# Performance work log

Measured on AMD Instinct MI355X. Metric: run time of the kernel, lower is better.

## Reference

```python
import jax, jax.numpy as jnp
import numpy as np

SQ, B, H, D = 2048, 1, 16, 64
HIDDEN = H * D


def setup_inputs() -> dict:
    key = jax.random.key(0)
    kq, kk, kv = jax.random.split(key, 3)
    query_layer = jax.random.normal(kq, (SQ, B, H, D), dtype=jnp.float32)
    key_layer = jax.random.normal(kk, (SQ, B, H, D), dtype=jnp.float32)
    value_layer = jax.random.normal(kv, (SQ, B, H, D), dtype=jnp.float32)
    return {"query_layer": query_layer, "key_layer": key_layer, "value_layer": value_layer}


def reference(query_layer, key_layer, value_layer):
    sq, b, h, d = query_layer.shape
    sk = key_layer.shape[0]
    norm = 1.0 / jnp.sqrt(jnp.asarray(d, dtype=query_layer.dtype))
    # scores: [b, h, sq, sk]  (materialized in the original via baddbmm)
    scores = jnp.einsum('sbhd,tbhd->bhst', query_layer, key_layer) * norm
    # causal mask (tril over [sq, sk]); masked positions -> -10000.0 as in original
    causal = jnp.tril(jnp.ones((sq, sk), dtype=bool))
    scores = jnp.where(causal[None, None], scores, jnp.asarray(-10000.0, scores.dtype))
    probs = jax.nn.softmax(scores, axis=-1)
    # context: [sq, b, h, d] -> [sq, b, hidden]
    ctx = jnp.einsum('bhst,tbhd->sbhd', probs, value_layer)
    return ctx.reshape(sq, b, h * d)
```

## Files before the change

kernel.cpp:

```cpp
#include <hip/hip_runtime.h>

typedef __bf16 bf16_t;
typedef bf16_t bf16x4 __attribute__((ext_vector_type(4)));
typedef bf16_t bf16x8 __attribute__((ext_vector_type(8)));
typedef float f32x4 __attribute__((ext_vector_type(4)));

namespace {
constexpr int kSQ = 2048;
constexpr int kNH = 16;
constexpr int kHD = 64;
constexpr int kHID = kNH * kHD;
constexpr int kBM = 64;
constexpr int kBN = 64;
constexpr int kPitch = 72;
constexpr int kNM = kSQ / kBM;
}

__global__ __launch_bounds__(256, 2)
void fattn_kernel(const float* __restrict__ Qg, const float* __restrict__ Kg,
                  const float* __restrict__ Vg, float* __restrict__ Og) {
  __shared__ __align__(16) bf16_t qs[kBM * kPitch];
  __shared__ __align__(16) bf16_t ks[kBN * kPitch];
  __shared__ __align__(16) bf16_t vt[kHD * kPitch];
  __shared__ __align__(16) bf16_t ps[4 * 16 * kPitch];

  const int bid  = blockIdx.x;
  const int head = bid & (kNH - 1);
  const int idx  = (bid >> 4) & 15;
  const int mblk = (bid < 256) ? (31 - idx) : idx;
  const int m0   = mblk * kBM;

  const int tid  = threadIdx.x;
  const int wave = tid >> 6;
  const int lane = tid & 63;
  const int quad = lane >> 4;
  const int lc   = lane & 15;
  const int wrow = wave * 16;

  const float kQScale = 0.125f * 1.44269504088896340736f;

  #pragma unroll
  for (int i = 0; i < 4; ++i) {
    const int v   = tid + 256 * i;
    const int row = v >> 4;
    const int c4  = (v & 15) * 4;
    const float4 f = *(const float4*)(Qg + (size_t)(m0 + row) * kHID + head * kHD + c4);
    bf16x4 h;
    h[0] = (bf16_t)(f.x * kQScale);
    h[1] = (bf16_t)(f.y * kQScale);
    h[2] = (bf16_t)(f.z * kQScale);
    h[3] = (bf16_t)(f.w * kQScale);
    *(bf16x4*)(qs + row * kPitch + c4) = h;
  }

  f32x4 acc[4];
  #pragma unroll
  for (int d16 = 0; d16 < 4; ++d16) acc[d16] = (f32x4){0.f, 0.f, 0.f, 0.f};
  float lacc[4] = {0.f, 0.f, 0.f, 0.f};

  bf16_t* psw = ps + wave * 16 * kPitch;

  float4 kreg[4];
  float  vreg[16];

  const int krow[4] = { (tid + 0) >> 4, (tid + 256) >> 4, (tid + 512) >> 4, (tid + 768) >> 4 };
  const int kc4 = (tid & 15) * 4;

  auto load_tile = [&](int kv0) {
    #pragma unroll
    for (int i = 0; i < 4; ++i)
      kreg[i] = *(const float4*)(Kg + (size_t)(kv0 + krow[i]) * kHID + head * kHD + kc4);
    #pragma unroll
    for (int i = 0; i < 4; ++i)
      #pragma unroll
      for (int k = 0; k < 4; ++k)
        vreg[i * 4 + k] = Vg[(size_t)(kv0 + wrow + i * 4 + k) * kHID + head * kHD + lane];
  };

  auto store_tile = [&]() {
    #pragma unroll
    for (int i = 0; i < 4; ++i) {
      bf16x4 hk;
      hk[0] = (bf16_t)kreg[i].x; hk[1] = (bf16_t)kreg[i].y;
      hk[2] = (bf16_t)kreg[i].z; hk[3] = (bf16_t)kreg[i].w;
      *(bf16x4*)(ks + krow[i] * kPitch + kc4) = hk;
      bf16x4 hv;
      hv[0] = (bf16_t)vreg[i * 4 + 0]; hv[1] = (bf16_t)vreg[i * 4 + 1];
      hv[2] = (bf16_t)vreg[i * 4 + 2]; hv[3] = (bf16_t)vreg[i * 4 + 3];
      *(bf16x4*)(vt + lane * kPitch + wrow + i * 4) = hv;
    }
  };

  load_tile(0);

  for (int j = 0; j <= mblk; ++j) {
    const int kv0 = j * kBN;
    __syncthreads();
    store_tile();
    __syncthreads();
    if (j < mblk) load_tile(kv0 + kBN);

    f32x4 s[4];
    #pragma unroll
    for (int n = 0; n < 4; ++n) {
      f32x4 cs = (f32x4){0.f, 0.f, 0.f, 0.f};
      #pragma unroll
      for (int kk = 0; kk < 2; ++kk) {
        bf16x8 a = *(const bf16x8*)(qs + (wrow + lc) * kPitch + kk * 32 + quad * 8);
        bf16x8 b = *(const bf16x8*)(ks + (n * 16 + lc) * kPitch + kk * 32 + quad * 8);
        cs = __builtin_amdgcn_mfma_f32_16x16x32_bf16(a, b, cs, 0, 0, 0);
      }
      s[n] = cs;
    }

    #pragma unroll
    for (int r = 0; r < 4; ++r) {
      const int grow = m0 + wrow + quad * 4 + r;
      #pragma unroll
      for (int n = 0; n < 4; ++n) {
        const int gcol = kv0 + n * 16 + lc;
        const float x = (gcol <= grow) ? s[n][r] : -1e30f;
        const float p = __builtin_amdgcn_exp2f(x);
        lacc[r] += p;
        psw[(quad * 4 + r) * kPitch + n * 16 + lc] = (bf16_t)p;
      }
    }

    #pragma unroll
    for (int kk = 0; kk < 2; ++kk) {
      bf16x8 a = *(const bf16x8*)(psw + lc * kPitch + kk * 32 + quad * 8);
      #pragma unroll
      for (int d16 = 0; d16 < 4; ++d16) {
        bf16x8 b = *(const bf16x8*)(vt + (d16 * 16 + lc) * kPitch + kk * 32 + quad * 8);
        acc[d16] = __builtin_amdgcn_mfma_f32_16x16x32_bf16(a, b, acc[d16], 0, 0, 0);
      }
    }
  }

  #pragma unroll
  for (int r = 0; r < 4; ++r) {
    float lsum = lacc[r];
    #pragma unroll
    for (int off = 1; off < 16; off <<= 1)
      lsum += __shfl_xor(lsum, off, 64);
    const float inv = 1.f / lsum;
    const int grow = m0 + wrow + quad * 4 + r;
    float* dst = Og + (size_t)grow * kHID + head * kHD;
    #pragma unroll
    for (int d16 = 0; d16 < 4; ++d16)
      dst[d16 * 16 + lc] = acc[d16][r] * inv;
  }
}

extern "C" void kernel_launch(void* const* d_in, const int* in_sizes, int n_in,
                              void* d_out, int out_size, void* d_ws, size_t ws_size,
                              hipStream_t stream) {
  (void)in_sizes; (void)n_in; (void)d_ws; (void)ws_size; (void)out_size;
  const float* Q = (const float*)d_in[0];
  const float* K = (const float*)d_in[1];
  const float* V = (const float*)d_in[2];
  float* O = (float*)d_out;
  dim3 grid(kNH * kNM);
  dim3 block(256);
  hipLaunchKernelGGL(fattn_kernel, grid, block, 0, stream, Q, K, V, O);
}
```

Before: 106.6 us.

## Split KV loop across two wave groups per block and merge partials in LDS

Doubles the block to 512 threads and splits it into two groups of four waves. The groups take alternating 64-wide KV tiles, each with its own K/V LDS buffers, and their partial outputs and row sums are merged through shared memory at the end. This shortens the serial KV loop per block and raises wave-level parallelism. It also applies the causal mask only on the diagonal tile and writes P as vectorized bf16x4 with a matching permuted V layout. In exchange, LDS use per block grows and an extra reduction pass plus synchronizations are added at the end.

```diff
diff --git a/kernel.cpp b/kernel.cpp
--- a/kernel.cpp
+++ b/kernel.cpp
@@ -6,42 +6,49 @@
 typedef float f32x4 __attribute__((ext_vector_type(4)));
 
 namespace {
-constexpr int kSQ = 2048;
 constexpr int kNH = 16;
 constexpr int kHD = 64;
 constexpr int kHID = kNH * kHD;
-constexpr int kBM = 64;
-constexpr int kBN = 64;
-constexpr int kPitch = 72;
-constexpr int kNM = kSQ / kBM;
+constexpr int kP = 72;
+constexpr int oQS  = 0;
+constexpr int oKS0 = 64 * kP;
+constexpr int oVT0 = oKS0 + 64 * kP;
+constexpr int oKS1 = oVT0 + 64 * kP;
+constexpr int oVT1 = oKS1 + 64 * kP;
+constexpr int oPS  = oVT1 + 64 * kP;
+constexpr int kSmemElems = oPS + 8 * 16 * kP;
 }
 
-__global__ __launch_bounds__(256, 2)
+__global__ __launch_bounds__(512, 4)
 void fattn_kernel(const float* __restrict__ Qg, const float* __restrict__ Kg,
                   const float* __restrict__ Vg, float* __restrict__ Og) {
-  __shared__ __align__(16) bf16_t qs[kBM * kPitch];
-  __shared__ __align__(16) bf16_t ks[kBN * kPitch];
-  __shared__ __align__(16) bf16_t vt[kHD * kPitch];
-  __shared__ __align__(16) bf16_t ps[4 * 16 * kPitch];
+  __shared__ __align__(16) bf16_t sm[kSmemElems];
 
   const int bid  = blockIdx.x;
   const int head = bid & (kNH - 1);
   const int idx  = (bid >> 4) & 15;
   const int mblk = (bid < 256) ? (31 - idx) : idx;
-  const int m0   = mblk * kBM;
+  const int m0   = mblk * 64;
 
   const int tid  = threadIdx.x;
   const int wave = tid >> 6;
   const int lane = tid & 63;
   const int quad = lane >> 4;
   const int lc   = lane & 15;
-  const int wrow = wave * 16;
+  const int g    = wave >> 2;
+  const int wg   = wave & 3;
+  const int wrow = wg * 16;
+
+  bf16_t* qs  = sm + oQS;
+  bf16_t* ks  = sm + (g ? oKS1 : oKS0);
+  bf16_t* vt  = sm + (g ? oVT1 : oVT0);
+  bf16_t* psw = sm + oPS + wave * 16 * kP;
 
   const float kQScale = 0.125f * 1.44269504088896340736f;
 
   #pragma unroll
-  for (int i = 0; i < 4; ++i) {
-    const int v   = tid + 256 * i;
+  for (int i = 0; i < 2; ++i) {
+    const int v   = tid + 512 * i;
     const int row = v >> 4;
     const int c4  = (v & 15) * 4;
     const float4 f = *(const float4*)(Qg + (size_t)(m0 + row) * kHID + head * kHD + c4);
@@ -50,7 +57,7 @@
     h[1] = (bf16_t)(f.y * kQScale);
     h[2] = (bf16_t)(f.z * kQScale);
     h[3] = (bf16_t)(f.w * kQScale);
-    *(bf16x4*)(qs + row * kPitch + c4) = h;
+    *(bf16x4*)(qs + row * kP + c4) = h;
   }
 
   f32x4 acc[4];
@@ -58,14 +65,15 @@
   for (int d16 = 0; d16 < 4; ++d16) acc[d16] = (f32x4){0.f, 0.f, 0.f, 0.f};
   float lacc[4] = {0.f, 0.f, 0.f, 0.f};
 
-  bf16_t* psw = ps + wave * 16 * kPitch;
+  const int tg  = wg * 64 + lane;
+  const int kc4 = (tg & 15) * 4;
+  int krow[4];
+  #pragma unroll
+  for (int i = 0; i < 4; ++i) krow[i] = (tg + 256 * i) >> 4;
 
   float4 kreg[4];
   float  vreg[16];
 
-  const int krow[4] = { (tid + 0) >> 4, (tid + 256) >> 4, (tid + 512) >> 4, (tid + 768) >> 4 };
-  const int kc4 = (tid & 15) * 4;
-
   auto load_tile = [&](int kv0) {
     #pragma unroll
     for (int i = 0; i < 4; ++i)
@@ -73,8 +81,8 @@
     #pragma unroll
     for (int i = 0; i < 4; ++i)
       #pragma unroll
-      for (int k = 0; k < 4; ++k)
-        vreg[i * 4 + k] = Vg[(size_t)(kv0 + wrow + i * 4 + k) * kHID + head * kHD + lane];
+      for (int n = 0; n < 4; ++n)
+        vreg[i * 4 + n] = Vg[(size_t)(kv0 + n * 16 + wg * 4 + i) * kHID + head * kHD + lane];
   };
 
   auto store_tile = [&]() {
@@ -83,22 +91,26 @@
       bf16x4 hk;
       hk[0] = (bf16_t)kreg[i].x; hk[1] = (bf16_t)kreg[i].y;
       hk[2] = (bf16_t)kreg[i].z; hk[3] = (bf16_t)kreg[i].w;
-      *(bf16x4*)(ks + krow[i] * kPitch + kc4) = hk;
+      *(bf16x4*)(ks + krow[i] * kP + kc4) = hk;
       bf16x4 hv;
       hv[0] = (bf16_t)vreg[i * 4 + 0]; hv[1] = (bf16_t)vreg[i * 4 + 1];
       hv[2] = (bf16_t)vreg[i * 4 + 2]; hv[3] = (bf16_t)vreg[i * 4 + 3];
-      *(bf16x4*)(vt + lane * kPitch + wrow + i * 4) = hv;
+      *(bf16x4*)(vt + lane * kP + (wg * 4 + i) * 4) = hv;
     }
   };
 
-  load_tile(0);
-
-  for (int j = 0; j <= mblk; ++j) {
-    const int kv0 = j * kBN;
+  if (g <= mblk) load_tile(g * 64);
+  const int Tmax = (mblk + 2) >> 1;
+
+  for (int t = 0; t < Tmax; ++t) {
+    const int j = 2 * t + g;
+    const bool active = (j <= mblk);
+    const int kv0 = j * 64;
     __syncthreads();
-    store_tile();
+    if (active) store_tile();
     __syncthreads();
-    if (j < mblk) load_tile(kv0 + kBN);
+    if (!active) continue;
+    if (j + 2 <= mblk) load_tile(kv0 + 128);
 
     f32x4 s[4];
     #pragma unroll
@@ -106,49 +118,81 @@
       f32x4 cs = (f32x4){0.f, 0.f, 0.f, 0.f};
       #pragma unroll
       for (int kk = 0; kk < 2; ++kk) {
-        bf16x8 a = *(const bf16x8*)(qs + (wrow + lc) * kPitch + kk * 32 + quad * 8);
-        bf16x8 b = *(const bf16x8*)(ks + (n * 16 + lc) * kPitch + kk * 32 + quad * 8);
+        bf16x8 a = *(const bf16x8*)(qs + (wrow + lc) * kP + kk * 32 + quad * 8);
+        bf16x8 b = *(const bf16x8*)(ks + (n * 16 + lc) * kP + kk * 32 + quad * 8);
         cs = __builtin_amdgcn_mfma_f32_16x16x32_bf16(a, b, cs, 0, 0, 0);
       }
       s[n] = cs;
     }
 
+    if (j == mblk) {
+      #pragma unroll
+      for (int r = 0; r < 4; ++r) {
+        const int grow = m0 + wrow + quad * 4 + r;
+        bf16x4 p4;
+        #pragma unroll
+        for (int n = 0; n < 4; ++n) {
+          const int gcol = kv0 + n * 16 + lc;
+          const float x = (gcol <= grow) ? s[n][r] : -1e30f;
+          const float p = __builtin_amdgcn_exp2f(x);
+          lacc[r] += p;
+          p4[n] = (bf16_t)p;
+        }
+        *(bf16x4*)(psw + (quad * 4 + r) * kP + lc * 4) = p4;
+      }
+    } else {
+      #pragma unroll
+      for (int r = 0; r < 4; ++r) {
+        bf16x4 p4;
+        #pragma unroll
+        for (int n = 0; n < 4; ++n) {
+          const float p = __builtin_amdgcn_exp2f(s[n][r]);
+          lacc[r] += p;
+          p4[n] = (bf16_t)p;
+        }
+        *(bf16x4*)(psw + (quad * 4 + r) * kP + lc * 4) = p4;
+      }
+    }
+
+    #pragma unroll
+    for (int kk = 0; kk < 2; ++kk) {
+      bf16x8 a = *(const bf16x8*)(psw + lc * kP + kk * 32 + quad * 8);
+      #pragma unroll
+      for (int d16 = 0; d16 < 4; ++d16) {
+        bf16x8 b = *(const bf16x8*)(vt + (d16 * 16 + lc) * kP + kk * 32 + quad * 8);
+        acc[d16] = __builtin_amdgcn_mfma_f32_16x16x32_bf16(a, b, acc[d16], 0, 0, 0);
+      }
+    }
+  }
+
+  __syncthreads();
+  float* mg = (float*)(sm + oKS1);
+  float* ml = (float*)(sm + oPS);
+  if (g == 1) {
     #pragma unroll
     for (int r = 0; r < 4; ++r) {
-      const int grow = m0 + wrow + quad * 4 + r;
-      #pragma unroll
-      for (int n = 0; n < 4; ++n) {
-        const int gcol = kv0 + n * 16 + lc;
-        const float x = (gcol <= grow) ? s[n][r] : -1e30f;
-        const float p = __builtin_amdgcn_exp2f(x);
-        lacc[r] += p;
-        psw[(quad * 4 + r) * kPitch + n * 16 + lc] = (bf16_t)p;
-      }
-    }
-
-    #pragma unroll
-    for (int kk = 0; kk < 2; ++kk) {
-      bf16x8 a = *(const bf16x8*)(psw + lc * kPitch + kk * 32 + quad * 8);
-      #pragma unroll
-      for (int d16 = 0; d16 < 4; ++d16) {
-        bf16x8 b = *(const bf16x8*)(vt + (d16 * 16 + lc) * kPitch + kk * 32 + quad * 8);
-        acc[d16] = __builtin_amdgcn_mfma_f32_16x16x32_bf16(a, b, acc[d16], 0, 0, 0);
-      }
-    }
-  }
-
-  #pragma unroll
-  for (int r = 0; r < 4; ++r) {
-    float lsum = lacc[r];
-    #pragma unroll
-    for (int off = 1; off < 16; off <<= 1)
-      lsum += __shfl_xor(lsum, off, 64);
-    const float inv = 1.f / lsum;
-    const int grow = m0 + wrow + quad * 4 + r;
-    float* dst = Og + (size_t)grow * kHID + head * kHD;
-    #pragma unroll
-    for (int d16 = 0; d16 < 4; ++d16)
-      dst[d16 * 16 + lc] = acc[d16][r] * inv;
+      const int row = wrow + quad * 4 + r;
+      #pragma unroll
+      for (int d16 = 0; d16 < 4; ++d16)
+        mg[row * 64 + d16 * 16 + lc] = acc[d16][r];
+      ml[row * 16 + lc] = lacc[r];
+    }
+  }
+  __syncthreads();
+  if (g == 0) {
+    #pragma unroll
+    for (int r = 0; r < 4; ++r) {
+      const int row = wrow + quad * 4 + r;
+      float lsum = lacc[r] + ml[row * 16 + lc];
+      #pragma unroll
+      for (int off = 1; off < 16; off <<= 1)
+        lsum += __shfl_xor(lsum, off, 64);
+      const float inv = 1.f / lsum;
+      float* dst = Og + (size_t)(m0 + row) * kHID + head * kHD;
+      #pragma unroll
+      for (int d16 = 0; d16 < 4; ++d16)
+        dst[d16 * 16 + lc] = (acc[d16][r] + mg[row * 64 + d16 * 16 + lc]) * inv;
+    }
   }
 }
 
@@ -160,7 +204,7 @@
   const float* K = (const float*)d_in[1];
   const float* V = (const float*)d_in[2];
   float* O = (float*)d_out;
-  dim3 grid(kNH * kNM);
-  dim3 block(256);
+  dim3 grid(512);
+  dim3 block(512);
   hipLaunchKernelGGL(fattn_kernel, grid, block, 0, stream, Q, K, V, O);
 }
```

After: 98.95 us. 1.08x faster.

## Split KV loop across waves with 32x32 MFMA and cross-wave output reduction

Applied to the files above, without the earlier changes.

Each block now handles a 32-row query tile, and its four waves each take every fourth KV tile independently (split-K within the block). Q is held in registers, K goes straight from registers into 32x32x16 MFMAs, and only V passes through per-wave shared memory, which removes the per-tile __syncthreads barriers. Partial outputs and row sums are reduced across waves through shared memory at the end. The grid doubles to 1024 blocks with occupancy hint 3, in exchange for redundant K/V global reads per block and an extra reduction step.

```diff
diff --git a/kernel.cpp b/kernel.cpp
--- a/kernel.cpp
+++ b/kernel.cpp
@@ -4,152 +4,177 @@
 typedef bf16_t bf16x4 __attribute__((ext_vector_type(4)));
 typedef bf16_t bf16x8 __attribute__((ext_vector_type(8)));
 typedef float f32x4 __attribute__((ext_vector_type(4)));
+typedef float f32x16 __attribute__((ext_vector_type(16)));
 
 namespace {
-constexpr int kSQ = 2048;
-constexpr int kNH = 16;
-constexpr int kHD = 64;
+constexpr int kNH  = 16;
+constexpr int kHD  = 64;
 constexpr int kHID = kNH * kHD;
-constexpr int kBM = 64;
-constexpr int kBN = 64;
-constexpr int kPitch = 72;
-constexpr int kNM = kSQ / kBM;
+constexpr int kVP  = 72;
+constexpr int kSmElems = 4 * 64 * kVP;
+constexpr int kOmPitch = 68;
 }
 
-__global__ __launch_bounds__(256, 2)
+__device__ __forceinline__ bf16x8 pack8(float4 a, float4 b) {
+  bf16x8 r;
+  r[0] = (bf16_t)a.x; r[1] = (bf16_t)a.y; r[2] = (bf16_t)a.z; r[3] = (bf16_t)a.w;
+  r[4] = (bf16_t)b.x; r[5] = (bf16_t)b.y; r[6] = (bf16_t)b.z; r[7] = (bf16_t)b.w;
+  return r;
+}
+
+__global__ __launch_bounds__(256, 3)
 void fattn_kernel(const float* __restrict__ Qg, const float* __restrict__ Kg,
                   const float* __restrict__ Vg, float* __restrict__ Og) {
-  __shared__ __align__(16) bf16_t qs[kBM * kPitch];
-  __shared__ __align__(16) bf16_t ks[kBN * kPitch];
-  __shared__ __align__(16) bf16_t vt[kHD * kPitch];
-  __shared__ __align__(16) bf16_t ps[4 * 16 * kPitch];
+  __shared__ __align__(16) bf16_t sm[kSmElems];
 
   const int bid  = blockIdx.x;
   const int head = bid & (kNH - 1);
-  const int idx  = (bid >> 4) & 15;
-  const int mblk = (bid < 256) ? (31 - idx) : idx;
-  const int m0   = mblk * kBM;
+  const int mt   = 63 - (bid >> 4);
+  const int m0   = mt * 32;
 
   const int tid  = threadIdx.x;
   const int wave = tid >> 6;
   const int lane = tid & 63;
-  const int quad = lane >> 4;
-  const int lc   = lane & 15;
-  const int wrow = wave * 16;
+  const int h    = lane >> 5;
+  const int m31  = lane & 31;
+
+  bf16_t* vt = sm + wave * 64 * kVP;
 
   const float kQScale = 0.125f * 1.44269504088896340736f;
 
-  #pragma unroll
-  for (int i = 0; i < 4; ++i) {
-    const int v   = tid + 256 * i;
-    const int row = v >> 4;
-    const int c4  = (v & 15) * 4;
-    const float4 f = *(const float4*)(Qg + (size_t)(m0 + row) * kHID + head * kHD + c4);
-    bf16x4 h;
-    h[0] = (bf16_t)(f.x * kQScale);
-    h[1] = (bf16_t)(f.y * kQScale);
-    h[2] = (bf16_t)(f.z * kQScale);
-    h[3] = (bf16_t)(f.w * kQScale);
-    *(bf16x4*)(qs + row * kPitch + c4) = h;
+  bf16x8 qf[4];
+  {
+    const float* qrow = Qg + (size_t)(m0 + m31) * kHID + head * kHD + h * 8;
+    #pragma unroll
+    for (int t = 0; t < 4; ++t) {
+      float4 a = *(const float4*)(qrow + 16 * t);
+      float4 b = *(const float4*)(qrow + 16 * t + 4);
+      a.x *= kQScale; a.y *= kQScale; a.z *= kQScale; a.w *= kQScale;
+      b.x *= kQScale; b.y *= kQScale; b.z *= kQScale; b.w *= kQScale;
+      qf[t] = pack8(a, b);
+    }
   }
 
-  f32x4 acc[4];
+  f32x16 Oa0, Oa1;
   #pragma unroll
-  for (int d16 = 0; d16 < 4; ++d16) acc[d16] = (f32x4){0.f, 0.f, 0.f, 0.f};
-  float lacc[4] = {0.f, 0.f, 0.f, 0.f};
+  for (int r = 0; r < 16; ++r) { Oa0[r] = 0.f; Oa1[r] = 0.f; }
+  float lacc = 0.f;
 
-  bf16_t* psw = ps + wave * 16 * kPitch;
+  const int kbase[8] = {0, 8, 4, 12, 16, 24, 20, 28};
 
-  float4 kreg[4];
-  float  vreg[16];
+  for (int jt = wave; jt <= mt; jt += 4) {
+    const int kv0 = jt * 32;
 
-  const int krow[4] = { (tid + 0) >> 4, (tid + 256) >> 4, (tid + 512) >> 4, (tid + 768) >> 4 };
-  const int kc4 = (tid & 15) * 4;
+    float vv[32];
+    const float* vbase = Vg + (size_t)kv0 * kHID + head * kHD + lane;
+    #pragma unroll
+    for (int q = 0; q < 8; ++q)
+      #pragma unroll
+      for (int t = 0; t < 4; ++t)
+        vv[q * 4 + t] = vbase[(size_t)(kbase[q] + t) * kHID];
 
-  auto load_tile = [&](int kv0) {
+    const float* krow = Kg + (size_t)(kv0 + m31) * kHID + head * kHD + h * 8;
+    float4 ka[4], kb[4];
     #pragma unroll
-    for (int i = 0; i < 4; ++i)
-      kreg[i] = *(const float4*)(Kg + (size_t)(kv0 + krow[i]) * kHID + head * kHD + kc4);
-    #pragma unroll
-    for (int i = 0; i < 4; ++i)
-      #pragma unroll
-      for (int k = 0; k < 4; ++k)
-        vreg[i * 4 + k] = Vg[(size_t)(kv0 + wrow + i * 4 + k) * kHID + head * kHD + lane];
-  };
-
-  auto store_tile = [&]() {
-    #pragma unroll
-    for (int i = 0; i < 4; ++i) {
-      bf16x4 hk;
-      hk[0] = (bf16_t)kreg[i].x; hk[1] = (bf16_t)kreg[i].y;
-      hk[2] = (bf16_t)kreg[i].z; hk[3] = (bf16_t)kreg[i].w;
-      *(bf16x4*)(ks + krow[i] * kPitch + kc4) = hk;
-      bf16x4 hv;
-      hv[0] = (bf16_t)vreg[i * 4 + 0]; hv[1] = (bf16_t)vreg[i * 4 + 1];
-      hv[2] = (bf16_t)vreg[i * 4 + 2]; hv[3] = (bf16_t)vreg[i * 4 + 3];
-      *(bf16x4*)(vt + lane * kPitch + wrow + i * 4) = hv;
-    }
-  };
-
-  load_tile(0);
-
-  for (int j = 0; j <= mblk; ++j) {
-    const int kv0 = j * kBN;
-    __syncthreads();
-    store_tile();
-    __syncthreads();
-    if (j < mblk) load_tile(kv0 + kBN);
-
-    f32x4 s[4];
-    #pragma unroll
-    for (int n = 0; n < 4; ++n) {
-      f32x4 cs = (f32x4){0.f, 0.f, 0.f, 0.f};
-      #pragma unroll
-      for (int kk = 0; kk < 2; ++kk) {
-        bf16x8 a = *(const bf16x8*)(qs + (wrow + lc) * kPitch + kk * 32 + quad * 8);
-        bf16x8 b = *(const bf16x8*)(ks + (n * 16 + lc) * kPitch + kk * 32 + quad * 8);
-        cs = __builtin_amdgcn_mfma_f32_16x16x32_bf16(a, b, cs, 0, 0, 0);
-      }
-      s[n] = cs;
+    for (int t = 0; t < 4; ++t) {
+      ka[t] = *(const float4*)(krow + 16 * t);
+      kb[t] = *(const float4*)(krow + 16 * t + 4);
     }
 
     #pragma unroll
-    for (int r = 0; r < 4; ++r) {
-      const int grow = m0 + wrow + quad * 4 + r;
+    for (int q = 0; q < 8; ++q) {
+      bf16x4 hv;
+      hv[0] = (bf16_t)vv[q * 4 + 0]; hv[1] = (bf16_t)vv[q * 4 + 1];
+      hv[2] = (bf16_t)vv[q * 4 + 2]; hv[3] = (bf16_t)vv[q * 4 + 3];
+      *(bf16x4*)(vt + lane * kVP + q * 4) = hv;
+    }
+
+    f32x16 cs;
+    #pragma unroll
+    for (int r = 0; r < 16; ++r) cs[r] = 0.f;
+    #pragma unroll
+    for (int t = 0; t < 4; ++t) {
+      bf16x8 af = pack8(ka[t], kb[t]);
+      cs = __builtin_amdgcn_mfma_f32_32x32x16_bf16(af, qf[t], cs, 0, 0, 0);
+    }
+
+    float p[16];
+    if (jt == mt) {
       #pragma unroll
-      for (int n = 0; n < 4; ++n) {
-        const int gcol = kv0 + n * 16 + lc;
-        const float x = (gcol <= grow) ? s[n][r] : -1e30f;
-        const float p = __builtin_amdgcn_exp2f(x);
-        lacc[r] += p;
-        psw[(quad * 4 + r) * kPitch + n * 16 + lc] = (bf16_t)p;
+      for (int r = 0; r < 16; ++r) {
+        const int kr = (r & 3) + 8 * (r >> 2) + 4 * h;
+        const float x = __builtin_amdgcn_exp2f(cs[r]);
+        p[r] = (kr <= m31) ? x : 0.f;
+        lacc += p[r];
+      }
+    } else {
+      #pragma unroll
+      for (int r = 0; r < 16; ++r) {
+        p[r] = __builtin_amdgcn_exp2f(cs[r]);
+        lacc += p[r];
       }
     }
 
+    bf16x8 pb0, pb1;
     #pragma unroll
-    for (int kk = 0; kk < 2; ++kk) {
-      bf16x8 a = *(const bf16x8*)(psw + lc * kPitch + kk * 32 + quad * 8);
-      #pragma unroll
-      for (int d16 = 0; d16 < 4; ++d16) {
-        bf16x8 b = *(const bf16x8*)(vt + (d16 * 16 + lc) * kPitch + kk * 32 + quad * 8);
-        acc[d16] = __builtin_amdgcn_mfma_f32_16x16x32_bf16(a, b, acc[d16], 0, 0, 0);
-      }
+    for (int j = 0; j < 8; ++j) { pb0[j] = (bf16_t)p[j]; pb1[j] = (bf16_t)p[8 + j]; }
+
+    {
+      bf16x8 va00 = *(const bf16x8*)(vt + (size_t)m31 * kVP + 8 * h);
+      bf16x8 va01 = *(const bf16x8*)(vt + (size_t)m31 * kVP + 16 + 8 * h);
+      bf16x8 va10 = *(const bf16x8*)(vt + (size_t)(32 + m31) * kVP + 8 * h);
+      bf16x8 va11 = *(const bf16x8*)(vt + (size_t)(32 + m31) * kVP + 16 + 8 * h);
+      Oa0 = __builtin_amdgcn_mfma_f32_32x32x16_bf16(va00, pb0, Oa0, 0, 0, 0);
+      Oa1 = __builtin_amdgcn_mfma_f32_32x32x16_bf16(va10, pb0, Oa1, 0, 0, 0);
+      Oa0 = __builtin_amdgcn_mfma_f32_32x32x16_bf16(va01, pb1, Oa0, 0, 0, 0);
+      Oa1 = __builtin_amdgcn_mfma_f32_32x32x16_bf16(va11, pb1, Oa1, 0, 0, 0);
     }
   }
 
+  __syncthreads();
+  float* fv   = (float*)sm;
+  float* Om   = fv + wave * 32 * kOmPitch;
+  float* larr = fv + 4 * 32 * kOmPitch;
+
   #pragma unroll
-  for (int r = 0; r < 4; ++r) {
-    float lsum = lacc[r];
+  for (int md = 0; md < 2; ++md) {
+    const f32x16& Oa = md ? Oa1 : Oa0;
     #pragma unroll
-    for (int off = 1; off < 16; off <<= 1)
-      lsum += __shfl_xor(lsum, off, 64);
-    const float inv = 1.f / lsum;
-    const int grow = m0 + wrow + quad * 4 + r;
-    float* dst = Og + (size_t)grow * kHID + head * kHD;
+    for (int q = 0; q < 4; ++q) {
+      f32x4 v;
+      v[0] = Oa[4 * q + 0]; v[1] = Oa[4 * q + 1];
+      v[2] = Oa[4 * q + 2]; v[3] = Oa[4 * q + 3];
+      *(f32x4*)(Om + (size_t)m31 * kOmPitch + 32 * md + 8 * q + 4 * h) = v;
+    }
+  }
+  larr[wave * 64 + lane] = lacc;
+  __syncthreads();
+
+  const int row = tid >> 3;
+  const int c0  = (tid & 7) * 8;
+  float l = 0.f;
+  #pragma unroll
+  for (int w = 0; w < 4; ++w)
+    l += larr[w * 64 + row] + larr[w * 64 + row + 32];
+  const float inv = 1.f / l;
+
+  f32x4 o0, o1;
+  #pragma unroll
+  for (int e = 0; e < 4; ++e) { o0[e] = 0.f; o1[e] = 0.f; }
+  #pragma unroll
+  for (int w = 0; w < 4; ++w) {
+    const float* src = fv + w * 32 * kOmPitch + (size_t)row * kOmPitch + c0;
+    f32x4 a = *(const f32x4*)(src);
+    f32x4 b = *(const f32x4*)(src + 4);
     #pragma unroll
-    for (int d16 = 0; d16 < 4; ++d16)
-      dst[d16 * 16 + lc] = acc[d16][r] * inv;
+    for (int e = 0; e < 4; ++e) { o0[e] += a[e]; o1[e] += b[e]; }
   }
+  #pragma unroll
+  for (int e = 0; e < 4; ++e) { o0[e] *= inv; o1[e] *= inv; }
+
+  float* dst = Og + (size_t)(m0 + row) * kHID + head * kHD + c0;
+  *(f32x4*)(dst)     = o0;
+  *(f32x4*)(dst + 4) = o1;
 }
 
 extern "C" void kernel_launch(void* const* d_in, const int* in_sizes, int n_in,
@@ -160,7 +185,7 @@
   const float* K = (const float*)d_in[1];
   const float* V = (const float*)d_in[2];
   float* O = (float*)d_out;
-  dim3 grid(kNH * kNM);
+  dim3 grid(1024);
   dim3 block(256);
   hipLaunchKernelGGL(fattn_kernel, grid, block, 0, stream, Q, K, V, O);
 }
```

Result: slower. 119.6 us (+12.2%).
